# Kernel tuning notes

Measured on AMD Instinct MI355X. Metric: run time of the kernel, lower is better.

The kernel has to match this reference:

```python
import jax, jax.numpy as jnp
import numpy as np

N_NODES = 200000
N_EDGES = 600000
IN_DIM = 130   # hidden_dim + 2
HID = 128
BN_EPS = 1e-5


def setup_inputs() -> dict:
    key = jax.random.key(0)
    ks = jax.random.split(key, 12)
    s = 0.05
    inp = {
        'x': jax.random.normal(ks[0], (N_NODES, IN_DIM), dtype=jnp.float32),
        'edge_index': jax.random.randint(ks[1], (2, N_EDGES), 0, N_NODES, dtype=jnp.int32),
        # SAGEConv 1: lin_l (aggregated neighbors, with bias), lin_r (root, no bias)
        'W1_l': jax.random.normal(ks[2], (IN_DIM, HID), dtype=jnp.float32) * s,
        'b1_l': jnp.zeros((HID,), dtype=jnp.float32),
        'W1_r': jax.random.normal(ks[3], (IN_DIM, HID), dtype=jnp.float32) * s,
        # BatchNorm1d(128) params + running stats (eval mode)
        'g1': jnp.ones((HID,), dtype=jnp.float32),
        'be1': jnp.zeros((HID,), dtype=jnp.float32),
        'rm1': jax.random.normal(ks[4], (HID,), dtype=jnp.float32) * 0.01,
        'rv1': jnp.ones((HID,), dtype=jnp.float32),
        # SAGEConv 2
        'W2_l': jax.random.normal(ks[5], (HID, HID), dtype=jnp.float32) * s,
        'b2_l': jnp.zeros((HID,), dtype=jnp.float32),
        'W2_r': jax.random.normal(ks[6], (HID, HID), dtype=jnp.float32) * s,
        'g2': jnp.ones((HID,), dtype=jnp.float32),
        'be2': jnp.zeros((HID,), dtype=jnp.float32),
        'rm2': jax.random.normal(ks[7], (HID,), dtype=jnp.float32) * 0.01,
        'rv2': jnp.ones((HID,), dtype=jnp.float32),
    }
    return inp


def _sage_mean(x, src, dst, W_l, b_l, W_r, n_nodes):
    # PyG SAGEConv (mean aggr): out = lin_l(mean_{j in N(i)} x_j) + lin_r(x_i)
    msg = x[src]                                                 # [E, F] gather
    agg = jax.ops.segment_sum(msg, dst, num_segments=n_nodes)    # [N, F]
    deg = jax.ops.segment_sum(jnp.ones((src.shape[0], 1), x.dtype), dst,
                              num_segments=n_nodes)              # [N, 1]
    mean = agg / jnp.maximum(deg, 1.0)
    return mean @ W_l + b_l + x @ W_r


def _bn_eval(x, g, b, rm, rv):
    return (x - rm) * (g * jax.lax.rsqrt(rv + BN_EPS)) + b


def reference(x, edge_index, W1_l, b1_l, W1_r, g1, be1, rm1, rv1,
              W2_l, b2_l, W2_r, g2, be2, rm2, rv2):
    src, dst = edge_index[0], edge_index[1]
    n = x.shape[0]
    h = _sage_mean(x, src, dst, W1_l, b1_l, W1_r, n)
    h = jax.nn.relu(_bn_eval(h, g1, be1, rm1, rv1))
    # dropout is identity in eval mode
    h = _sage_mean(h, src, dst, W2_l, b2_l, W2_r, n)
    h = jax.nn.relu(_bn_eval(h, g2, be2, rm2, rv2))
    return h
```

## Files before the change

### kernel.cpp

```cpp
#include <hip/hip_runtime.h>

typedef short v8s __attribute__((ext_vector_type(8)));
typedef float v4f __attribute__((ext_vector_type(4)));

__device__ __forceinline__ unsigned short f2bf(float x) {
  union { float f; unsigned int u; } c; c.f = x;
  unsigned int u = c.u;
  return (unsigned short)((u + 0x7fffu + ((u >> 16) & 1u)) >> 16);
}
__device__ __forceinline__ float bf2f(unsigned int hi16) {
  union { unsigned int u; float f; } c; c.u = hi16 << 16;
  return c.f;
}
__device__ __forceinline__ ushort2 pk(float2 v) {
  ushort2 p; p.x = f2bf(v.x); p.y = f2bf(v.y); return p;
}

#define ASTR 272
#define XSTR 136

__global__ void bn_fold_k(const float* __restrict__ g1, const float* __restrict__ be1,
                          const float* __restrict__ rm1, const float* __restrict__ rv1,
                          const float* __restrict__ g2, const float* __restrict__ be2,
                          const float* __restrict__ rm2, const float* __restrict__ rv2,
                          float* __restrict__ s1, float* __restrict__ t1,
                          float* __restrict__ s2, float* __restrict__ t2) {
  int i = threadIdx.x;
  if (i < 128) {
    float sv = g1[i] * rsqrtf(rv1[i] + 1e-5f);
    s1[i] = sv; t1[i] = be1[i] - rm1[i] * sv;
    float sw = g2[i] * rsqrtf(rv2[i] + 1e-5f);
    s2[i] = sw; t2[i] = be2[i] - rm2[i] * sw;
  }
}

template<int F, int XOFF, int KC>
__global__ void pack_w_k(const float* __restrict__ Wl, const float* __restrict__ Wr,
                         unsigned short* __restrict__ wpk) {
  int i = blockIdx.x * 256 + threadIdx.x;
  if (i >= KC * 4096) return;
  int kk = i & 31, n = (i >> 5) & 127, kc = i >> 12;
  int k = kc * 32 + kk;
  float v = 0.f;
  if (k < F) v = Wl[k * 128 + n];
  else if (k >= XOFF && k < XOFF + F) v = Wr[(k - XOFF) * 128 + n];
  wpk[i] = f2bf(v);
}

__global__ __launch_bounds__(256) void xb_k(const float* __restrict__ x,
                                            unsigned short* __restrict__ xb,
                                            unsigned short* __restrict__ A, int N) {
  const int r = threadIdx.x >> 6, l = threadIdx.x & 63;
  const int node = blockIdx.x * 4 + r;
  if (node > N) return;
  if (node == N) {
    *(unsigned int*)(xb + (long)node * XSTR + 2 * l) = 0u;
    if (l < 4) *(unsigned int*)(xb + (long)node * XSTR + 128 + 2 * l) = 0u;
    *(unsigned int*)(A + (long)node * ASTR + 136 + 2 * l) = 0u;
    return;
  }
  const float2* xr = (const float2*)(x + (long)node * 130);
  float2 v = xr[l];
  *(ushort2*)(xb + (long)node * XSTR + 2 * l) = pk(v);
  if (l == 0) { float2 w = xr[64]; *(ushort2*)(xb + (long)node * XSTR + 128) = pk(w); }
  if (l >= 1 && l < 4) *(unsigned int*)(xb + (long)node * XSTR + 128 + 2 * l) = 0u;
}

__global__ void zero_i_k(int* __restrict__ p, int n) {
  int i = blockIdx.x * 256 + threadIdx.x;
  if (i < n) p[i] = 0;
}
__global__ void count_k(const int* __restrict__ dst, int* __restrict__ degi, int E) {
  int i = blockIdx.x * 256 + threadIdx.x;
  if (i < E) atomicAdd(&degi[dst[i]], 1);
}
__global__ __launch_bounds__(256) void scan1_k(const int* __restrict__ degi,
                                               int* __restrict__ rowptr,
                                               int* __restrict__ bsum, int N) {
  __shared__ int sd[256];
  const int t = threadIdx.x;
  const int base = blockIdx.x * 1024 + t * 4;
  int v[4];
#pragma unroll
  for (int j = 0; j < 4; ++j) v[j] = (base + j < N) ? degi[base + j] : 0;
  const int tot = v[0] + v[1] + v[2] + v[3];
  sd[t] = tot;
  __syncthreads();
  for (int off = 1; off < 256; off <<= 1) {
    int o = (t >= off) ? sd[t - off] : 0;
    __syncthreads();
    sd[t] += o;
    __syncthreads();
  }
  int e = sd[t] - tot;
#pragma unroll
  for (int j = 0; j < 4; ++j) {
    if (base + j < N) rowptr[base + j] = e;
    e += v[j];
  }
  if (t == 255) bsum[blockIdx.x] = sd[255];
}
__global__ __launch_bounds__(256) void scan2_k(int* __restrict__ bsum, int nb) {
  __shared__ int sd[256];
  const int t = threadIdx.x;
  const int v = (t < nb) ? bsum[t] : 0;
  sd[t] = v;
  __syncthreads();
  for (int off = 1; off < 256; off <<= 1) {
    int o = (t >= off) ? sd[t - off] : 0;
    __syncthreads();
    sd[t] += o;
    __syncthreads();
  }
  if (t < nb) bsum[t] = sd[t] - v;
}
__global__ void scan3_k(int* __restrict__ rowptr, int* __restrict__ cursor,
                        const int* __restrict__ bsum, int N, int E) {
  int i = blockIdx.x * 256 + threadIdx.x;
  if (i < N) {
    int v = rowptr[i] + bsum[i >> 10];
    rowptr[i] = v;
    cursor[i] = v;
  } else if (i == N) {
    rowptr[N] = E;
  }
}
__global__ void fill_k(const int* __restrict__ src, const int* __restrict__ dst,
                       int* __restrict__ cursor, int* __restrict__ nbr, int E) {
  int i = blockIdx.x * 256 + threadIdx.x;
  if (i < E) {
    int p = atomicAdd(&cursor[dst[i]], 1);
    nbr[p] = src[i];
  }
}

template<int SSTR, int SOFF, bool EXTRA>
__global__ __launch_bounds__(256) void spmm_k(const unsigned short* __restrict__ src,
                                              const int* __restrict__ rowptr,
                                              const int* __restrict__ nbr,
                                              unsigned short* __restrict__ A, int N) {
  constexpr int JCH = EXTRA ? 4 : 8;
  const int w = threadIdx.x >> 6, lane = threadIdx.x & 63;
  const int nb = blockIdx.x * 16 + w * 4;
  if (nb >= N) return;

  int rp = 0;
  if (lane <= 4 && nb + lane <= N) rp = rowptr[nb + lane];
  int d[4], r0[4], myn[4];
  float2 a[4], b[4];
#pragma unroll
  for (int r = 0; r < 4; ++r) {
    r0[r] = __shfl(rp, r, 64);
    const int r1 = __shfl(rp, r + 1, 64);
    d[r] = (nb + r < N) ? (r1 - r0[r]) : 0;
    a[r] = make_float2(0.f, 0.f);
    b[r] = make_float2(0.f, 0.f);
    myn[r] = N;
    if (lane < min(d[r], 64)) myn[r] = nbr[r0[r] + lane];
  }
  const int dm = max(max(d[0], d[1]), max(d[2], d[3]));

  if (dm <= 64) {
    for (int e0 = 0; e0 < dm; e0 += JCH) {
      unsigned int u[4][JCH], wv[4][JCH];
#pragma unroll
      for (int j = 0; j < JCH; ++j) {
#pragma unroll
        for (int r = 0; r < 4; ++r) {
          const int e = e0 + j;
          const int idx = (e < d[r]) ? __shfl(myn[r], e, 64) : N;
          const unsigned short* p = src + (long)idx * SSTR + SOFF;
          u[r][j] = *(const unsigned int*)(p + 2 * lane);
          if (EXTRA) wv[r][j] = *(const unsigned int*)(p + 128);
        }
      }
#pragma unroll
      for (int r = 0; r < 4; ++r)
#pragma unroll
        for (int j = 0; j < JCH; ++j) {
          a[r].x += bf2f(u[r][j] & 0xffffu);
          a[r].y += bf2f(u[r][j] >> 16);
          if (EXTRA) {
            b[r].x += bf2f(wv[r][j] & 0xffffu);
            b[r].y += bf2f(wv[r][j] >> 16);
          }
        }
    }
  } else {
    for (int r = 0; r < 4; ++r) {
      for (int base = r0[r]; base < r0[r] + d[r]; base += 64) {
        const int cnt = min(64, r0[r] + d[r] - base);
        const int mn = (lane < cnt) ? nbr[base + lane] : N;
        for (int e = 0; e < cnt; ++e) {
          const unsigned short* p = src + (long)__shfl(mn, e, 64) * SSTR + SOFF;
          const unsigned int uu = *(const unsigned int*)(p + 2 * lane);
          a[r].x += bf2f(uu & 0xffffu);
          a[r].y += bf2f(uu >> 16);
          if (EXTRA) {
            const unsigned int ww = *(const unsigned int*)(p + 128);
            b[r].x += bf2f(ww & 0xffffu);
            b[r].y += bf2f(ww >> 16);
          }
        }
      }
    }
  }

#pragma unroll
  for (int r = 0; r < 4; ++r) {
    if (nb + r < N) {
      const float inv = 1.0f / fmaxf((float)d[r], 1.0f);
      float2 m; m.x = a[r].x * inv; m.y = a[r].y * inv;
      unsigned short* Ar = A + (long)(nb + r) * ASTR;
      *(ushort2*)(Ar + 2 * lane) = pk(m);
      if (EXTRA) {
        if (lane == 0) {
          float2 mb; mb.x = b[r].x * inv; mb.y = b[r].y * inv;
          *(ushort2*)(Ar + 128) = pk(mb);
        }
        if (lane >= 1 && lane < 4) *(unsigned int*)(Ar + 128 + 2 * lane) = 0u;
      }
    }
  }
}

template<int KC, int C0, int C1, int ST0, int ST1, bool L2MODE>
__global__ __launch_bounds__(256) void gemm_k(
    const unsigned short* __restrict__ S0, const unsigned short* __restrict__ S1,
    const unsigned short* __restrict__ wpk, const float* __restrict__ bias,
    const float* __restrict__ sc, const float* __restrict__ tc,
    void* __restrict__ out, int N) {
  constexpr int KP = KC * 32;
  constexpr int LDA = KP + 8;
  __shared__ __align__(16) unsigned short a_s[64][LDA];
  const int tid = threadIdx.x;
  const int node0 = blockIdx.x * 64;

  {
    const int row = tid >> 2, t4 = tid & 3;
    const int node = node0 + row;
#pragma unroll
    for (int i = 0; i < KC; ++i) {
      const int c = t4 + 4 * i;
      v8s v = {0, 0, 0, 0, 0, 0, 0, 0};
      if (node < N) {
        if (c < C0) v = *(const v8s*)(S0 + (long)node * ST0 + 8 * c);
        else if (c < C0 + C1) v = *(const v8s*)(S1 + (long)node * ST1 + 8 * (c - C0));
      }
      *(v8s*)&a_s[row][c * 8] = v;
    }
  }
  __syncthreads();

  const int wave = tid >> 6, lane = tid & 63;
  const int quad = lane >> 4, l16 = lane & 15;
  const int nt0 = wave * 2;
  v4f acc[4][2];
#pragma unroll
  for (int mt = 0; mt < 4; ++mt)
#pragma unroll
    for (int nt = 0; nt < 2; ++nt) acc[mt][nt] = (v4f){0.f, 0.f, 0.f, 0.f};

#pragma unroll
  for (int kc = 0; kc < KC; ++kc) {
    v8s bf[2];
#pragma unroll
    for (int nt = 0; nt < 2; ++nt) {
      const int n = (nt0 + nt) * 16 + l16;
      bf[nt] = *(const v8s*)(wpk + kc * 4096 + n * 32 + quad * 8);
    }
#pragma unroll
    for (int mt = 0; mt < 4; ++mt) {
      v8s af = *(const v8s*)(&a_s[mt * 16 + l16][kc * 32 + quad * 8]);
      acc[mt][0] = __builtin_amdgcn_mfma_f32_16x16x32_bf16(af, bf[0], acc[mt][0], 0, 0, 0);
      acc[mt][1] = __builtin_amdgcn_mfma_f32_16x16x32_bf16(af, bf[1], acc[mt][1], 0, 0, 0);
    }
  }

#pragma unroll
  for (int nt = 0; nt < 2; ++nt) {
    const int col = (nt0 + nt) * 16 + l16;
    const float bj = bias[col], sj = sc[col], tj = tc[col];
#pragma unroll
    for (int mt = 0; mt < 4; ++mt) {
#pragma unroll
      for (int r = 0; r < 4; ++r) {
        const int row = node0 + mt * 16 + quad * 4 + r;
        if (row < N) {
          float v = fmaxf((acc[mt][nt][r] + bj) * sj + tj, 0.f);
          if (L2MODE) ((float*)out)[(long)row * 128 + col] = v;
          else ((unsigned short*)out)[(long)row * ASTR + 136 + col] = f2bf(v);
        }
      }
    }
  }
}

extern "C" void kernel_launch(void* const* d_in, const int* in_sizes, int n_in,
                              void* d_out, int out_size, void* d_ws, size_t ws_size,
                              hipStream_t stream) {
  const float* x   = (const float*)d_in[0];
  const int*   ei  = (const int*)d_in[1];
  const float* W1l = (const float*)d_in[2];
  const float* b1  = (const float*)d_in[3];
  const float* W1r = (const float*)d_in[4];
  const float* g1  = (const float*)d_in[5];
  const float* be1 = (const float*)d_in[6];
  const float* rm1 = (const float*)d_in[7];
  const float* rv1 = (const float*)d_in[8];
  const float* W2l = (const float*)d_in[9];
  const float* b2  = (const float*)d_in[10];
  const float* W2r = (const float*)d_in[11];
  const float* g2  = (const float*)d_in[12];
  const float* be2 = (const float*)d_in[13];
  const float* rm2 = (const float*)d_in[14];
  const float* rv2 = (const float*)d_in[15];

  const int E = in_sizes[1] / 2;
  const int N = in_sizes[0] / 130;
  const int* src = ei;
  const int* dst = ei + E;

  unsigned short* A  = (unsigned short*)d_ws;
  unsigned short* xb = A + (size_t)(N + 1) * ASTR;
  unsigned short* wpk1 = xb + (size_t)(N + 1) * XSTR;
  unsigned short* wpk2 = wpk1 + 9 * 4096;
  float* s1 = (float*)(wpk2 + 8 * 4096);
  float* t1 = s1 + 128;
  float* s2 = t1 + 128;
  float* t2 = s2 + 128;
  int* degi   = (int*)(t2 + 128);
  int* rowptr = degi + N;
  int* bsum   = rowptr + N + 1;
  int* nbr    = bsum + 256;

  hipLaunchKernelGGL(bn_fold_k, dim3(1), dim3(128), 0, stream,
                     g1, be1, rm1, rv1, g2, be2, rm2, rv2, s1, t1, s2, t2);
  hipLaunchKernelGGL((pack_w_k<130, 136, 9>), dim3(144), dim3(256), 0, stream, W1l, W1r, wpk1);
  hipLaunchKernelGGL((pack_w_k<128, 128, 8>), dim3(128), dim3(256), 0, stream, W2l, W2r, wpk2);
  hipLaunchKernelGGL(xb_k, dim3((N + 4) / 4), dim3(256), 0, stream, x, xb, A, N);

  hipLaunchKernelGGL(zero_i_k, dim3((N + 255) / 256), dim3(256), 0, stream, degi, N);
  hipLaunchKernelGGL(count_k, dim3((E + 255) / 256), dim3(256), 0, stream, dst, degi, E);
  const int nb = (N + 1023) / 1024;
  hipLaunchKernelGGL(scan1_k, dim3(nb), dim3(256), 0, stream, degi, rowptr, bsum, N);
  hipLaunchKernelGGL(scan2_k, dim3(1), dim3(256), 0, stream, bsum, nb);
  hipLaunchKernelGGL(scan3_k, dim3((N + 256) / 256), dim3(256), 0, stream,
                     rowptr, degi, bsum, N, E);
  hipLaunchKernelGGL(fill_k, dim3((E + 255) / 256), dim3(256), 0, stream,
                     src, dst, degi, nbr, E);

  const int nsb = (N + 15) / 16;
  const int ngb = (N + 63) / 64;

  hipLaunchKernelGGL((spmm_k<XSTR, 0, true>), dim3(nsb), dim3(256), 0, stream,
                     xb, rowptr, nbr, A, N);
  hipLaunchKernelGGL((gemm_k<9, 17, 17, ASTR, XSTR, false>), dim3(ngb), dim3(256), 0, stream,
                     A, xb, wpk1, b1, s1, t1, (void*)A, N);
  hipLaunchKernelGGL((spmm_k<ASTR, 136, false>), dim3(nsb), dim3(256), 0, stream,
                     A, rowptr, nbr, A, N);
  hipLaunchKernelGGL((gemm_k<8, 16, 16, ASTR, ASTR, true>), dim3(ngb), dim3(256), 0, stream,
                     A, A + 136, wpk2, b2, s2, t2, d_out, N);
}
```

Baseline: 511.3 us.

## Reorder SAGE layers to transform-then-aggregate with fused BN/ReLU epilogue

Uses linearity of the mean to apply W_l and W_r first in one GEMM producing two 128-wide projections, then gathers and averages the projected rows and adds the root term, bias-folded BN and ReLU in the SpMM epilogue. This removes the separate x-to-bf16 conversion kernel, shrinks the K dimension of the GEMM, and narrows gathered rows from 130+ to 128 columns. The first GEMM now reads fp32 x directly, and the intermediate is rounded to bf16 before aggregation, which changes rounding behaviour.

```diff
diff --git a/kernel.cpp b/kernel.cpp
--- a/kernel.cpp
+++ b/kernel.cpp
@@ -16,54 +16,35 @@
   ushort2 p; p.x = f2bf(v.x); p.y = f2bf(v.y); return p;
 }
 
-#define ASTR 272
-#define XSTR 136
-
 __global__ void bn_fold_k(const float* __restrict__ g1, const float* __restrict__ be1,
                           const float* __restrict__ rm1, const float* __restrict__ rv1,
+                          const float* __restrict__ b1,
                           const float* __restrict__ g2, const float* __restrict__ be2,
                           const float* __restrict__ rm2, const float* __restrict__ rv2,
+                          const float* __restrict__ b2,
                           float* __restrict__ s1, float* __restrict__ t1,
-                          float* __restrict__ s2, float* __restrict__ t2) {
+                          float* __restrict__ s2, float* __restrict__ t2,
+                          unsigned short* __restrict__ bufA, int N) {
   int i = threadIdx.x;
   if (i < 128) {
     float sv = g1[i] * rsqrtf(rv1[i] + 1e-5f);
-    s1[i] = sv; t1[i] = be1[i] - rm1[i] * sv;
+    s1[i] = sv; t1[i] = (b1[i] - rm1[i]) * sv + be1[i];
     float sw = g2[i] * rsqrtf(rv2[i] + 1e-5f);
-    s2[i] = sw; t2[i] = be2[i] - rm2[i] * sw;
-  }
-}
-
-template<int F, int XOFF, int KC>
-__global__ void pack_w_k(const float* __restrict__ Wl, const float* __restrict__ Wr,
-                         unsigned short* __restrict__ wpk) {
-  int i = blockIdx.x * 256 + threadIdx.x;
-  if (i >= KC * 4096) return;
-  int kk = i & 31, n = (i >> 5) & 127, kc = i >> 12;
+    s2[i] = sw; t2[i] = (b2[i] - rm2[i]) * sw + be2[i];
+  }
+  if (i < 64) ((unsigned int*)(bufA + (long)N * 128))[i] = 0u;
+}
+
+template<int K, int KC>
+__global__ void pack2_k(const float* __restrict__ Wl, const float* __restrict__ Wr,
+                        unsigned short* __restrict__ wpk) {
+  int i = blockIdx.x * 256 + threadIdx.x;
+  if (i >= KC * 8192) return;
+  int kk = i & 31, n = (i >> 5) & 255, kc = i >> 13;
   int k = kc * 32 + kk;
   float v = 0.f;
-  if (k < F) v = Wl[k * 128 + n];
-  else if (k >= XOFF && k < XOFF + F) v = Wr[(k - XOFF) * 128 + n];
+  if (k < K) v = (n < 128) ? Wl[k * 128 + n] : Wr[k * 128 + (n - 128)];
   wpk[i] = f2bf(v);
-}
-
-__global__ __launch_bounds__(256) void xb_k(const float* __restrict__ x,
-                                            unsigned short* __restrict__ xb,
-                                            unsigned short* __restrict__ A, int N) {
-  const int r = threadIdx.x >> 6, l = threadIdx.x & 63;
-  const int node = blockIdx.x * 4 + r;
-  if (node > N) return;
-  if (node == N) {
-    *(unsigned int*)(xb + (long)node * XSTR + 2 * l) = 0u;
-    if (l < 4) *(unsigned int*)(xb + (long)node * XSTR + 128 + 2 * l) = 0u;
-    *(unsigned int*)(A + (long)node * ASTR + 136 + 2 * l) = 0u;
-    return;
-  }
-  const float2* xr = (const float2*)(x + (long)node * 130);
-  float2 v = xr[l];
-  *(ushort2*)(xb + (long)node * XSTR + 2 * l) = pk(v);
-  if (l == 0) { float2 w = xr[64]; *(ushort2*)(xb + (long)node * XSTR + 128) = pk(w); }
-  if (l >= 1 && l < 4) *(unsigned int*)(xb + (long)node * XSTR + 128 + 2 * l) = 0u;
 }
 
 __global__ void zero_i_k(int* __restrict__ p, int n) {
@@ -134,12 +115,93 @@
   }
 }
 
-template<int SSTR, int SOFF, bool EXTRA>
-__global__ __launch_bounds__(256) void spmm_k(const unsigned short* __restrict__ src,
-                                              const int* __restrict__ rowptr,
-                                              const int* __restrict__ nbr,
-                                              unsigned short* __restrict__ A, int N) {
-  constexpr int JCH = EXTRA ? 4 : 8;
+template<int KC, bool SRCF32>
+__global__ __launch_bounds__(256) void gemm2_k(const void* __restrict__ Asrc,
+                                               const unsigned short* __restrict__ wpk,
+                                               unsigned short* __restrict__ Ol,
+                                               unsigned short* __restrict__ Or, int N) {
+  constexpr int KP = KC * 32;
+  constexpr int LDA = KP + 8;
+  __shared__ __align__(16) unsigned short a_s[64][LDA];
+  const int tid = threadIdx.x;
+  const int node0 = blockIdx.x * 64;
+  const int row = tid >> 2, t4 = tid & 3;
+  const int node = node0 + row;
+
+  if constexpr (SRCF32) {
+    const float* xr = (const float*)Asrc + (long)node * 130;
+#pragma unroll
+    for (int j = 0; j < 16; ++j) {
+      float2 v = make_float2(0.f, 0.f);
+      if (node < N) v = *(const float2*)(xr + 8 * j + 2 * t4);
+      *(ushort2*)&a_s[row][8 * j + 2 * t4] = pk(v);
+    }
+    v8s z = {0, 0, 0, 0, 0, 0, 0, 0};
+    if (t4 == 0 && node < N) {
+      float2 v = *(const float2*)(xr + 128);
+      z[0] = (short)f2bf(v.x); z[1] = (short)f2bf(v.y);
+    }
+    *(v8s*)&a_s[row][128 + t4 * 8] = z;
+  } else {
+    const unsigned short* hr = (const unsigned short*)Asrc + (long)node * 128;
+#pragma unroll
+    for (int i = 0; i < KC; ++i) {
+      const int c = t4 + 4 * i;
+      v8s v = {0, 0, 0, 0, 0, 0, 0, 0};
+      if (node < N) v = *(const v8s*)(hr + 8 * c);
+      *(v8s*)&a_s[row][c * 8] = v;
+    }
+  }
+  __syncthreads();
+
+  const int wave = tid >> 6, lane = tid & 63;
+  const int quad = lane >> 4, l16 = lane & 15;
+  v4f acc[4][4];
+#pragma unroll
+  for (int mt = 0; mt < 4; ++mt)
+#pragma unroll
+    for (int nt = 0; nt < 4; ++nt) acc[mt][nt] = (v4f){0.f, 0.f, 0.f, 0.f};
+
+  const unsigned short* wb = wpk + (wave * 64 + l16) * 32 + quad * 8;
+#pragma unroll
+  for (int kc = 0; kc < KC; ++kc) {
+    v8s bf[4];
+#pragma unroll
+    for (int nt = 0; nt < 4; ++nt)
+      bf[nt] = *(const v8s*)(wb + kc * 8192 + nt * 512);
+#pragma unroll
+    for (int mt = 0; mt < 4; ++mt) {
+      v8s af = *(const v8s*)(&a_s[mt * 16 + l16][kc * 32 + quad * 8]);
+#pragma unroll
+      for (int nt = 0; nt < 4; ++nt)
+        acc[mt][nt] = __builtin_amdgcn_mfma_f32_16x16x32_bf16(af, bf[nt], acc[mt][nt], 0, 0, 0);
+    }
+  }
+
+#pragma unroll
+  for (int nt = 0; nt < 4; ++nt) {
+    const int col = wave * 64 + nt * 16 + l16;
+    unsigned short* ob = (col < 128) ? Ol : Or;
+    const int oc = col & 127;
+#pragma unroll
+    for (int mt = 0; mt < 4; ++mt) {
+#pragma unroll
+      for (int r = 0; r < 4; ++r) {
+        const int rw = node0 + mt * 16 + quad * 4 + r;
+        if (rw < N) ob[(long)rw * 128 + oc] = f2bf(acc[mt][nt][r]);
+      }
+    }
+  }
+}
+
+template<bool OUTF32>
+__global__ __launch_bounds__(256) void spmm_f_k(const unsigned short* __restrict__ gsrc,
+                                                const unsigned short* __restrict__ rsrc,
+                                                const int* __restrict__ rowptr,
+                                                const int* __restrict__ nbr,
+                                                const float* __restrict__ sc,
+                                                const float* __restrict__ tc,
+                                                void* __restrict__ out, int N) {
   const int w = threadIdx.x >> 6, lane = threadIdx.x & 63;
   const int nb = blockIdx.x * 16 + w * 4;
   if (nb >= N) return;
@@ -147,43 +209,35 @@
   int rp = 0;
   if (lane <= 4 && nb + lane <= N) rp = rowptr[nb + lane];
   int d[4], r0[4], myn[4];
-  float2 a[4], b[4];
+  float2 a[4];
 #pragma unroll
   for (int r = 0; r < 4; ++r) {
     r0[r] = __shfl(rp, r, 64);
     const int r1 = __shfl(rp, r + 1, 64);
     d[r] = (nb + r < N) ? (r1 - r0[r]) : 0;
     a[r] = make_float2(0.f, 0.f);
-    b[r] = make_float2(0.f, 0.f);
     myn[r] = N;
     if (lane < min(d[r], 64)) myn[r] = nbr[r0[r] + lane];
   }
   const int dm = max(max(d[0], d[1]), max(d[2], d[3]));
 
   if (dm <= 64) {
-    for (int e0 = 0; e0 < dm; e0 += JCH) {
-      unsigned int u[4][JCH], wv[4][JCH];
-#pragma unroll
-      for (int j = 0; j < JCH; ++j) {
+    for (int e0 = 0; e0 < dm; e0 += 8) {
+      unsigned int u[4][8];
+#pragma unroll
+      for (int j = 0; j < 8; ++j)
 #pragma unroll
         for (int r = 0; r < 4; ++r) {
           const int e = e0 + j;
           const int idx = (e < d[r]) ? __shfl(myn[r], e, 64) : N;
-          const unsigned short* p = src + (long)idx * SSTR + SOFF;
-          u[r][j] = *(const unsigned int*)(p + 2 * lane);
-          if (EXTRA) wv[r][j] = *(const unsigned int*)(p + 128);
+          u[r][j] = *(const unsigned int*)(gsrc + (long)idx * 128 + 2 * lane);
         }
-      }
 #pragma unroll
       for (int r = 0; r < 4; ++r)
 #pragma unroll
-        for (int j = 0; j < JCH; ++j) {
+        for (int j = 0; j < 8; ++j) {
           a[r].x += bf2f(u[r][j] & 0xffffu);
           a[r].y += bf2f(u[r][j] >> 16);
-          if (EXTRA) {
-            b[r].x += bf2f(wv[r][j] & 0xffffu);
-            b[r].y += bf2f(wv[r][j] >> 16);
-          }
         }
     }
   } else {
@@ -192,105 +246,31 @@
         const int cnt = min(64, r0[r] + d[r] - base);
         const int mn = (lane < cnt) ? nbr[base + lane] : N;
         for (int e = 0; e < cnt; ++e) {
-          const unsigned short* p = src + (long)__shfl(mn, e, 64) * SSTR + SOFF;
-          const unsigned int uu = *(const unsigned int*)(p + 2 * lane);
+          const unsigned int uu =
+              *(const unsigned int*)(gsrc + (long)__shfl(mn, e, 64) * 128 + 2 * lane);
           a[r].x += bf2f(uu & 0xffffu);
           a[r].y += bf2f(uu >> 16);
-          if (EXTRA) {
-            const unsigned int ww = *(const unsigned int*)(p + 128);
-            b[r].x += bf2f(ww & 0xffffu);
-            b[r].y += bf2f(ww >> 16);
-          }
         }
       }
     }
   }
 
+  const float2 sv = *(const float2*)(sc + 2 * lane);
+  const float2 tv = *(const float2*)(tc + 2 * lane);
 #pragma unroll
   for (int r = 0; r < 4; ++r) {
     if (nb + r < N) {
       const float inv = 1.0f / fmaxf((float)d[r], 1.0f);
-      float2 m; m.x = a[r].x * inv; m.y = a[r].y * inv;
-      unsigned short* Ar = A + (long)(nb + r) * ASTR;
-      *(ushort2*)(Ar + 2 * lane) = pk(m);
-      if (EXTRA) {
-        if (lane == 0) {
-          float2 mb; mb.x = b[r].x * inv; mb.y = b[r].y * inv;
-          *(ushort2*)(Ar + 128) = pk(mb);
-        }
-        if (lane >= 1 && lane < 4) *(unsigned int*)(Ar + 128 + 2 * lane) = 0u;
-      }
-    }
-  }
-}
-
-template<int KC, int C0, int C1, int ST0, int ST1, bool L2MODE>
-__global__ __launch_bounds__(256) void gemm_k(
-    const unsigned short* __restrict__ S0, const unsigned short* __restrict__ S1,
-    const unsigned short* __restrict__ wpk, const float* __restrict__ bias,
-    const float* __restrict__ sc, const float* __restrict__ tc,
-    void* __restrict__ out, int N) {
-  constexpr int KP = KC * 32;
-  constexpr int LDA = KP + 8;
-  __shared__ __align__(16) unsigned short a_s[64][LDA];
-  const int tid = threadIdx.x;
-  const int node0 = blockIdx.x * 64;
-
-  {
-    const int row = tid >> 2, t4 = tid & 3;
-    const int node = node0 + row;
-#pragma unroll
-    for (int i = 0; i < KC; ++i) {
-      const int c = t4 + 4 * i;
-      v8s v = {0, 0, 0, 0, 0, 0, 0, 0};
-      if (node < N) {
-        if (c < C0) v = *(const v8s*)(S0 + (long)node * ST0 + 8 * c);
-        else if (c < C0 + C1) v = *(const v8s*)(S1 + (long)node * ST1 + 8 * (c - C0));
-      }
-      *(v8s*)&a_s[row][c * 8] = v;
-    }
-  }
-  __syncthreads();
-
-  const int wave = tid >> 6, lane = tid & 63;
-  const int quad = lane >> 4, l16 = lane & 15;
-  const int nt0 = wave * 2;
-  v4f acc[4][2];
-#pragma unroll
-  for (int mt = 0; mt < 4; ++mt)
-#pragma unroll
-    for (int nt = 0; nt < 2; ++nt) acc[mt][nt] = (v4f){0.f, 0.f, 0.f, 0.f};
-
-#pragma unroll
-  for (int kc = 0; kc < KC; ++kc) {
-    v8s bf[2];
-#pragma unroll
-    for (int nt = 0; nt < 2; ++nt) {
-      const int n = (nt0 + nt) * 16 + l16;
-      bf[nt] = *(const v8s*)(wpk + kc * 4096 + n * 32 + quad * 8);
-    }
-#pragma unroll
-    for (int mt = 0; mt < 4; ++mt) {
-      v8s af = *(const v8s*)(&a_s[mt * 16 + l16][kc * 32 + quad * 8]);
-      acc[mt][0] = __builtin_amdgcn_mfma_f32_16x16x32_bf16(af, bf[0], acc[mt][0], 0, 0, 0);
-      acc[mt][1] = __builtin_amdgcn_mfma_f32_16x16x32_bf16(af, bf[1], acc[mt][1], 0, 0, 0);
-    }
-  }
-
-#pragma unroll
-  for (int nt = 0; nt < 2; ++nt) {
-    const int col = (nt0 + nt) * 16 + l16;
-    const float bj = bias[col], sj = sc[col], tj = tc[col];
-#pragma unroll
-    for (int mt = 0; mt < 4; ++mt) {
-#pragma unroll
-      for (int r = 0; r < 4; ++r) {
-        const int row = node0 + mt * 16 + quad * 4 + r;
-        if (row < N) {
-          float v = fmaxf((acc[mt][nt][r] + bj) * sj + tj, 0.f);
-          if (L2MODE) ((float*)out)[(long)row * 128 + col] = v;
-          else ((unsigned short*)out)[(long)row * ASTR + 136 + col] = f2bf(v);
-        }
+      const unsigned int ur = *(const unsigned int*)(rsrc + (long)(nb + r) * 128 + 2 * lane);
+      float yx = a[r].x * inv + bf2f(ur & 0xffffu);
+      float yy = a[r].y * inv + bf2f(ur >> 16);
+      yx = fmaxf(yx * sv.x + tv.x, 0.f);
+      yy = fmaxf(yy * sv.y + tv.y, 0.f);
+      if (OUTF32) {
+        *(float2*)((float*)out + (long)(nb + r) * 128 + 2 * lane) = make_float2(yx, yy);
+      } else {
+        *(ushort2*)((unsigned short*)out + (long)(nb + r) * 128 + 2 * lane) =
+            pk(make_float2(yx, yy));
       }
     }
   }
@@ -321,11 +301,11 @@
   const int* src = ei;
   const int* dst = ei + E;
 
-  unsigned short* A  = (unsigned short*)d_ws;
-  unsigned short* xb = A + (size_t)(N + 1) * ASTR;
-  unsigned short* wpk1 = xb + (size_t)(N + 1) * XSTR;
-  unsigned short* wpk2 = wpk1 + 9 * 4096;
-  float* s1 = (float*)(wpk2 + 8 * 4096);
+  unsigned short* bufA = (unsigned short*)d_ws;
+  unsigned short* bufB = bufA + (size_t)(N + 1) * 128;
+  unsigned short* wpka = bufB + (size_t)(N + 1) * 128;
+  unsigned short* wpkb = wpka + 5 * 8192;
+  float* s1 = (float*)(wpkb + 4 * 8192);
   float* t1 = s1 + 128;
   float* s2 = t1 + 128;
   float* t2 = s2 + 128;
@@ -335,10 +315,10 @@
   int* nbr    = bsum + 256;
 
   hipLaunchKernelGGL(bn_fold_k, dim3(1), dim3(128), 0, stream,
-                     g1, be1, rm1, rv1, g2, be2, rm2, rv2, s1, t1, s2, t2);
-  hipLaunchKernelGGL((pack_w_k<130, 136, 9>), dim3(144), dim3(256), 0, stream, W1l, W1r, wpk1);
-  hipLaunchKernelGGL((pack_w_k<128, 128, 8>), dim3(128), dim3(256), 0, stream, W2l, W2r, wpk2);
-  hipLaunchKernelGGL(xb_k, dim3((N + 4) / 4), dim3(256), 0, stream, x, xb, A, N);
+                     g1, be1, rm1, rv1, b1, g2, be2, rm2, rv2, b2,
+                     s1, t1, s2, t2, bufA, N);
+  hipLaunchKernelGGL((pack2_k<130, 5>), dim3(160), dim3(256), 0, stream, W1l, W1r, wpka);
+  hipLaunchKernelGGL((pack2_k<128, 4>), dim3(128), dim3(256), 0, stream, W2l, W2r, wpkb);
 
   hipLaunchKernelGGL(zero_i_k, dim3((N + 255) / 256), dim3(256), 0, stream, degi, N);
   hipLaunchKernelGGL(count_k, dim3((E + 255) / 256), dim3(256), 0, stream, dst, degi, E);
@@ -350,15 +330,15 @@
   hipLaunchKernelGGL(fill_k, dim3((E + 255) / 256), dim3(256), 0, stream,
                      src, dst, degi, nbr, E);
 
+  const int ngb = (N + 63) / 64;
   const int nsb = (N + 15) / 16;
-  const int ngb = (N + 63) / 64;
-
-  hipLaunchKernelGGL((spmm_k<XSTR, 0, true>), dim3(nsb), dim3(256), 0, stream,
-                     xb, rowptr, nbr, A, N);
-  hipLaunchKernelGGL((gemm_k<9, 17, 17, ASTR, XSTR, false>), dim3(ngb), dim3(256), 0, stream,
-                     A, xb, wpk1, b1, s1, t1, (void*)A, N);
-  hipLaunchKernelGGL((spmm_k<ASTR, 136, false>), dim3(nsb), dim3(256), 0, stream,
-                     A, rowptr, nbr, A, N);
-  hipLaunchKernelGGL((gemm_k<8, 16, 16, ASTR, ASTR, true>), dim3(ngb), dim3(256), 0, stream,
-                     A, A + 136, wpk2, b2, s2, t2, d_out, N);
-}
+
+  hipLaunchKernelGGL((gemm2_k<5, true>), dim3(ngb), dim3(256), 0, stream,
+                     (const void*)x, wpka, bufA, bufB, N);
+  hipLaunchKernelGGL((spmm_f_k<false>), dim3(nsb), dim3(256), 0, stream,
+                     bufA, bufB, rowptr, nbr, s1, t1, (void*)bufB, N);
+  hipLaunchKernelGGL((gemm2_k<4, false>), dim3(ngb), dim3(256), 0, stream,
+                     (const void*)bufB, wpkb, bufA, bufB, N);
+  hipLaunchKernelGGL((spmm_f_k<true>), dim3(nsb), dim3(256), 0, stream,
+                     bufA, bufB, rowptr, nbr, s2, t2, d_out, N);
+}
```

Result: faster. 478.6 us (-6.4%).
